# Performance work log

Hardware: AMD Instinct MI355X
Metric: run time of the kernel (lower is better)

## Reference

```python
import jax, jax.numpy as jnp
import numpy as np

# ---- module constants (from init_kwargs) ----
NOF_LINKS = 64
NOISE = 1e-3          # gen_para.input_noise_power
DT = 0.01             # gen_para.dt
T_END = 5.12          # t
TXP = 1.0             # gen_para.tx_power
LAM = 1.0
RHO = 1.0

T_ARR = jnp.arange(0.0, T_END, DT, dtype=jnp.float32)   # [T] time grid
POW2T = jnp.power(jnp.float32(2.0), T_ARR)               # 2^t
POW2T_1 = POW2T - 1.0                                    # 2^t - 1
LN2 = jnp.log(jnp.float32(2.0))


def setup_inputs() -> dict:
    key = jax.random.key(0)
    k1, k2 = jax.random.split(key)
    pathloss = jax.random.uniform(k1, (NOF_LINKS, NOF_LINKS), dtype=jnp.float32)
    powers = jax.random.uniform(k2, (16, 20, NOF_LINKS), dtype=jnp.float32)
    return {"pathloss": pathloss, "powers": powers}


def _outage(pathloss, power):
    # power: [B, N, L]; pathloss: [L, L]
    B, N, L = power.shape
    T = T_ARR.shape[0]
    # signal[b,n,i,j] = pathloss[i,j] * power[b,n,i]  (per original expand/permute)
    y_ii = jnp.diagonal(pathloss)[None, None, :] * power              # [B,N,L]
    y_tot = power * jnp.sum(pathloss, axis=1)[None, None, :]          # sum_j signal
    y_ij = y_tot - y_ii
    sinr = y_ii / (y_ij + NOISE)                                      # [B,N,L]

    # block-0 outage CDF over time grid: Q1[b,i,t] = 1 - exp(-(2^t-1) * sinr[b,0,i])
    Q1 = 1.0 - jnp.exp(-POW2T_1[None, None, :] * sinr[:, 0, :, None])  # [B,L,T]

    # per-block pdf kernels for n >= 1 (vectorized over all blocks up front)
    s = sinr[:, 1:, :, None]                                          # [B,N-1,L,1]
    q = jnp.exp(-POW2T_1 * s) * POW2T * s * LN2                       # [B,N-1,L,T]

    def step(Q, qn):
        # Q, qn: [B,L,T]; per-channel grouped cross-correlation (torch conv1d semantics)
        x = Q.reshape(1, B * L, T)
        w = qn.reshape(B * L, 1, T)
        out = jax.lax.conv_general_dilated(
            x, w, window_strides=(1,), padding=[(T - 1, T - 1)],
            feature_group_count=B * L)                                 # [1,B*L,2T-1]
        Qn = out[0, :, :T].reshape(B, L, T) * DT
        return Qn, Qn[:, :, -1]

    q_scan = jnp.moveaxis(q, 1, 0)                                    # [N-1,B,L,T]
    _, outa_rest = jax.lax.scan(step, Q1, q_scan)                     # [N-1,B,L]
    outa = jnp.concatenate([Q1[None, :, :, -1], outa_rest], axis=0)   # [N,B,L]
    return jnp.moveaxis(outa, 0, 1)                                   # [B,N,L]


def reference(pathloss, powers):
    power = powers * TXP
    N = power.shape[1]
    outa = _outage(pathloss, power)                                   # [B,N,L]
    E = power[:, 0, :] + jnp.sum(power[:, 1:, :] * outa[:, :N - 1, :], axis=1)
    D = 1.0 + jnp.sum(outa[:, :N - 1, :], axis=1)
    loss = jnp.sum(E) + LAM * jnp.sum(outa[:, N - 1, :]) + RHO * jnp.sum(D)
    return loss
```

## Files before the change

### kernel.cpp

```cpp
#include <hip/hip_runtime.h>

#define LL 64
#define NN 20
#define DTC 0.01f
#define NOISEC 1e-3f
#define LN2C 0.69314718056f
#define LOG2E 1.44269504089f

typedef __attribute__((ext_vector_type(8))) short short8x;
typedef __attribute__((ext_vector_type(4))) float f32x4;

__device__ __forceinline__ unsigned cvt_pk_bf16(float x, float y) {
    unsigned r;
    asm("v_cvt_pk_bf16_f32 %0, %1, %2" : "=v"(r) : "v"(x), "v"(y));
    return r;
}

__global__ __launch_bounds__(64, 1) void outage_kernel(
    const float* __restrict__ pathloss,
    const float* __restrict__ powers,
    float* __restrict__ out)
{
    __shared__ __align__(16) unsigned short gt[2][8][544];
    __shared__ __align__(16) unsigned short Qb[2][1024];

    const int lane = threadIdx.x;
    const int c = blockIdx.x, b = c >> 6, l = c & 63;
    const int nh = lane & 15;
    const int qd = lane >> 4;

    const float pl = pathloss[l * LL + lane];
    float rs = pl;
    #pragma unroll
    for (int mk = 1; mk < 64; mk <<= 1) rs += __shfl_xor(rs, mk, 64);
    const float dg   = __shfl(pl, l, 64);
    const float dsum = rs - dg;

    float P2[8], P1L[8];
    #pragma unroll
    for (int u = 0; u < 8; ++u) {
        float e = __builtin_amdgcn_exp2f((8 * lane + u) * DTC);
        P2[u]  = e;
        P1L[u] = (1.f - e) * LOG2E;
    }

    *((uint4*)&Qb[0][0] + lane) = uint4{0u, 0u, 0u, 0u};
    *((uint4*)&Qb[1][0] + lane) = uint4{0u, 0u, 0u, 0u};
    {
        const int bb = lane >> 5, w = lane & 31;
        #pragma unroll
        for (int k = 0; k < 8; ++k) gt[bb][k][512 + w] = 0;
    }

    const float p0 = powers[(b * NN + 0) * LL + l];
    const float s0 = dg * p0 / (p0 * dsum + NOISEC);
    float q7;
    {
        float v[8];
        #pragma unroll
        for (int u = 0; u < 8; ++u) v[u] = 1.f - __builtin_amdgcn_exp2f(P1L[u] * s0);
        q7 = v[7];
        uint4 d4 = { cvt_pk_bf16(v[0], v[1]), cvt_pk_bf16(v[2], v[3]),
                     cvt_pk_bf16(v[4], v[5]), cvt_pk_bf16(v[6], v[7]) };
        *(uint4*)&Qb[0][512 + 8 * lane] = d4;
    }

    const float p1v = powers[(b * NN + 1) * LL + l];
    float lossCh = 1.f + p0 + (p1v + 1.f) * q7;

    auto fill_g = [&](int buf, float p) {
        float s  = dg * p / (p * dsum + NOISEC);
        float cm = s * LN2C * DTC;
        unsigned F[8];
        #pragma unroll
        for (int w = 0; w < 4; ++w) {
            float a  = __builtin_amdgcn_exp2f(P1L[2 * w]     * s) * (P2[2 * w]     * cm);
            float bb = __builtin_amdgcn_exp2f(P1L[2 * w + 1] * s) * (P2[2 * w + 1] * cm);
            F[w] = cvt_pk_bf16(a, bb);
        }
        #pragma unroll
        for (int w = 0; w < 4; ++w) {
            unsigned t = (unsigned)__shfl_down((int)F[w], 1, 64);
            F[4 + w] = (lane == 63) ? 0u : t;
        }
        unsigned E[7];
        #pragma unroll
        for (int j = 0; j < 7; ++j) E[j] = __builtin_amdgcn_alignbit(F[j + 1], F[j], 16);
        #pragma unroll
        for (int k = 0; k < 8; ++k) {
            uint4 d4;
            if ((k & 1) == 0) d4 = uint4{F[k / 2], F[k / 2 + 1], F[k / 2 + 2], F[k / 2 + 3]};
            else              d4 = uint4{E[k / 2], E[k / 2 + 1], E[k / 2 + 2], E[k / 2 + 3]};
            *(uint4*)&gt[buf][k][8 * lane] = d4;
        }
    };
    fill_g(1, p1v);

    const int kk    = (7 - nh) & 7;
    const int baseA = 511 - nh + 8 * qd - kk;
    const int baseB = 512 + 32 * nh + 8 * qd;
    const int dstw  = 512 + 32 * nh + 4 * qd;

    float pnext = powers[(b * NN + 2) * LL + l];

    short8x Bv[16], A0v[16], A1v[16];
    {
        const unsigned short* pg1 = &gt[1][kk][0];
        #pragma unroll
        for (int d = 0; d < 16; ++d) {
            Bv[d]  = *(const short8x*)&Qb[0][baseB - 32 * d];
            A0v[d] = *(const short8x*)&pg1[baseA - 32 * d];
            A1v[d] = *(const short8x*)&pg1[baseA - 32 * d - 16];
        }
    }

    for (int n = 1; n < NN; ++n) {
        unsigned short* pdst = &Qb[n & 1][0];

        float pfut = 0.f;
        if (n <= NN - 3) pfut = powers[(b * NN + n + 2) * LL + l];

        if (n < NN - 1) fill_g((n + 1) & 1, pnext);

        f32x4 acc0a = {0.f, 0.f, 0.f, 0.f}, acc0b = {0.f, 0.f, 0.f, 0.f};
        f32x4 acc1a = {0.f, 0.f, 0.f, 0.f}, acc1b = {0.f, 0.f, 0.f, 0.f};
        #pragma unroll
        for (int d = 0; d < 16; d += 2) {
            acc0a = __builtin_amdgcn_mfma_f32_16x16x32_bf16(A0v[d],     Bv[d],     acc0a, 0, 0, 0);
            acc1a = __builtin_amdgcn_mfma_f32_16x16x32_bf16(A1v[d],     Bv[d],     acc1a, 0, 0, 0);
            acc0b = __builtin_amdgcn_mfma_f32_16x16x32_bf16(A0v[d + 1], Bv[d + 1], acc0b, 0, 0, 0);
            acc1b = __builtin_amdgcn_mfma_f32_16x16x32_bf16(A1v[d + 1], Bv[d + 1], acc1b, 0, 0, 0);
        }
        f32x4 acc0 = acc0a + acc0b;
        f32x4 acc1 = acc1a + acc1b;

        *(uint2*)&pdst[dstw]      = uint2{cvt_pk_bf16(acc0.x, acc0.y), cvt_pk_bf16(acc0.z, acc0.w)};
        *(uint2*)&pdst[dstw + 16] = uint2{cvt_pk_bf16(acc1.x, acc1.y), cvt_pk_bf16(acc1.z, acc1.w)};

        if (n < NN - 1) {
            const unsigned short* pgn = &gt[(n + 1) & 1][kk][0];
            #pragma unroll
            for (int d = 0; d < 16; ++d) {
                Bv[d]  = *(const short8x*)&pdst[baseB - 32 * d];
                A0v[d] = *(const short8x*)&pgn[baseA - 32 * d];
                A1v[d] = *(const short8x*)&pgn[baseA - 32 * d - 16];
            }
        }

        float wgt = (n < NN - 1) ? (pnext + 1.f) : 1.f;
        lossCh += wgt * acc1.w;
        pnext = pfut;
    }

    if (lane == 63) atomicAdd(out, lossCh);
}

extern "C" void kernel_launch(void* const* d_in, const int* in_sizes, int n_in,
                              void* d_out, int out_size, void* d_ws, size_t ws_size,
                              hipStream_t stream) {
    const float* pathloss = (const float*)d_in[0];
    const float* powers   = (const float*)d_in[1];
    float* outp = (float*)d_out;

    (void)hipMemsetAsync(d_out, 0, sizeof(float) * out_size, stream);
    outage_kernel<<<16 * LL, 64, 0, stream>>>(pathloss, powers, outp);
}
```

Measured before the change: 85.93 us.

## Process two batches per wavefront and build shifted B operands via DPP

Each workgroup now handles two batch rows (b and b+8) for the same link, halving the grid and sharing the pathloss reduction and exponent tables. The two independent convolution chains are interleaved so MFMA work of one can overlap LDS loads and kernel fills of the other. Instead of loading 16 shifted B fragments from LDS, one fragment is loaded and the other 15 are produced with DPP row-shift-right operations, cutting LDS reads. It adds register pressure, and row-shift semantics must match the original 32-element-stride loads exactly or results change.

```diff
diff --git a/kernel.cpp b/kernel.cpp
--- a/kernel.cpp
+++ b/kernel.cpp
@@ -7,25 +7,57 @@
 #define LN2C 0.69314718056f
 #define LOG2E 1.44269504089f
 
+#define GROW 552
+
 typedef __attribute__((ext_vector_type(8))) short short8x;
 typedef __attribute__((ext_vector_type(4))) float f32x4;
+typedef __attribute__((ext_vector_type(4))) int v4i;
 
 __device__ __forceinline__ unsigned cvt_pk_bf16(float x, float y) {
     unsigned r;
     asm("v_cvt_pk_bf16_f32 %0, %1, %2" : "=v"(r) : "v"(x), "v"(y));
     return r;
 }
+
+template<int CTRL>
+__device__ __forceinline__ short8x dpp_shr(short8x v) {
+    v4i p = __builtin_bit_cast(v4i, v);
+    v4i q;
+    q.x = __builtin_amdgcn_update_dpp(0, p.x, CTRL, 0xf, 0xf, true);
+    q.y = __builtin_amdgcn_update_dpp(0, p.y, CTRL, 0xf, 0xf, true);
+    q.z = __builtin_amdgcn_update_dpp(0, p.z, CTRL, 0xf, 0xf, true);
+    q.w = __builtin_amdgcn_update_dpp(0, p.w, CTRL, 0xf, 0xf, true);
+    return __builtin_bit_cast(short8x, q);
+}
+
+#define DPP_EXPAND(B)                         \
+    B[1]  = dpp_shr<0x111>(B[0]);             \
+    B[2]  = dpp_shr<0x112>(B[0]);             \
+    B[3]  = dpp_shr<0x113>(B[0]);             \
+    B[4]  = dpp_shr<0x114>(B[0]);             \
+    B[5]  = dpp_shr<0x115>(B[0]);             \
+    B[6]  = dpp_shr<0x116>(B[0]);             \
+    B[7]  = dpp_shr<0x117>(B[0]);             \
+    B[8]  = dpp_shr<0x118>(B[0]);             \
+    B[9]  = dpp_shr<0x119>(B[0]);             \
+    B[10] = dpp_shr<0x11A>(B[0]);             \
+    B[11] = dpp_shr<0x11B>(B[0]);             \
+    B[12] = dpp_shr<0x11C>(B[0]);             \
+    B[13] = dpp_shr<0x11D>(B[0]);             \
+    B[14] = dpp_shr<0x11E>(B[0]);             \
+    B[15] = dpp_shr<0x11F>(B[0]);
 
 __global__ __launch_bounds__(64, 1) void outage_kernel(
     const float* __restrict__ pathloss,
     const float* __restrict__ powers,
     float* __restrict__ out)
 {
-    __shared__ __align__(16) unsigned short gt[2][8][544];
-    __shared__ __align__(16) unsigned short Qb[2][1024];
+    __shared__ __align__(16) unsigned short gt[2][2][8][GROW];
+    __shared__ __align__(16) unsigned short Qb[2][2][1024];
 
     const int lane = threadIdx.x;
-    const int c = blockIdx.x, b = c >> 6, l = c & 63;
+    const int c0 = blockIdx.x, b0 = c0 >> 6, l = c0 & 63;
+    const int b1 = b0 + 8;
     const int nh = lane & 15;
     const int qd = lane >> 4;
 
@@ -44,31 +76,43 @@
         P1L[u] = (1.f - e) * LOG2E;
     }
 
-    *((uint4*)&Qb[0][0] + lane) = uint4{0u, 0u, 0u, 0u};
-    *((uint4*)&Qb[1][0] + lane) = uint4{0u, 0u, 0u, 0u};
+    *((uint4*)&Qb[0][0][0] + lane) = uint4{0u, 0u, 0u, 0u};
+    *((uint4*)&Qb[0][1][0] + lane) = uint4{0u, 0u, 0u, 0u};
+    *((uint4*)&Qb[1][0][0] + lane) = uint4{0u, 0u, 0u, 0u};
+    *((uint4*)&Qb[1][1][0] + lane) = uint4{0u, 0u, 0u, 0u};
     {
         const int bb = lane >> 5, w = lane & 31;
         #pragma unroll
-        for (int k = 0; k < 8; ++k) gt[bb][k][512 + w] = 0;
-    }
-
-    const float p0 = powers[(b * NN + 0) * LL + l];
-    const float s0 = dg * p0 / (p0 * dsum + NOISEC);
-    float q7;
+        for (int k = 0; k < 8; ++k) { gt[0][bb][k][512 + w] = 0; gt[1][bb][k][512 + w] = 0; }
+    }
+
+    const float p00 = powers[(b0 * NN + 0) * LL + l];
+    const float p01 = powers[(b1 * NN + 0) * LL + l];
+    const float s00 = dg * p00 / (p00 * dsum + NOISEC);
+    const float s01 = dg * p01 / (p01 * dsum + NOISEC);
+    float q70, q71;
     {
-        float v[8];
-        #pragma unroll
-        for (int u = 0; u < 8; ++u) v[u] = 1.f - __builtin_amdgcn_exp2f(P1L[u] * s0);
-        q7 = v[7];
-        uint4 d4 = { cvt_pk_bf16(v[0], v[1]), cvt_pk_bf16(v[2], v[3]),
+        float v[8], w[8];
+        #pragma unroll
+        for (int u = 0; u < 8; ++u) {
+            v[u] = 1.f - __builtin_amdgcn_exp2f(P1L[u] * s00);
+            w[u] = 1.f - __builtin_amdgcn_exp2f(P1L[u] * s01);
+        }
+        q70 = v[7]; q71 = w[7];
+        uint4 d0 = { cvt_pk_bf16(v[0], v[1]), cvt_pk_bf16(v[2], v[3]),
                      cvt_pk_bf16(v[4], v[5]), cvt_pk_bf16(v[6], v[7]) };
-        *(uint4*)&Qb[0][512 + 8 * lane] = d4;
-    }
-
-    const float p1v = powers[(b * NN + 1) * LL + l];
-    float lossCh = 1.f + p0 + (p1v + 1.f) * q7;
-
-    auto fill_g = [&](int buf, float p) {
+        uint4 d1 = { cvt_pk_bf16(w[0], w[1]), cvt_pk_bf16(w[2], w[3]),
+                     cvt_pk_bf16(w[4], w[5]), cvt_pk_bf16(w[6], w[7]) };
+        *(uint4*)&Qb[0][0][512 + 8 * lane] = d0;
+        *(uint4*)&Qb[1][0][512 + 8 * lane] = d1;
+    }
+
+    const float p1v0 = powers[(b0 * NN + 1) * LL + l];
+    const float p1v1 = powers[(b1 * NN + 1) * LL + l];
+    float loss0 = 1.f + p00 + (p1v0 + 1.f) * q70;
+    float loss1 = 1.f + p01 + (p1v1 + 1.f) * q71;
+
+    auto fill_g = [&](unsigned short* gtb, float p) {
         float s  = dg * p / (p * dsum + NOISEC);
         float cm = s * LN2C * DTC;
         unsigned F[8];
@@ -91,68 +135,96 @@
             uint4 d4;
             if ((k & 1) == 0) d4 = uint4{F[k / 2], F[k / 2 + 1], F[k / 2 + 2], F[k / 2 + 3]};
             else              d4 = uint4{E[k / 2], E[k / 2 + 1], E[k / 2 + 2], E[k / 2 + 3]};
-            *(uint4*)&gt[buf][k][8 * lane] = d4;
+            *(uint4*)&gtb[k * GROW + 8 * lane] = d4;
         }
     };
-    fill_g(1, p1v);
+    fill_g(&gt[0][1][0][0], p1v0);
+    fill_g(&gt[1][1][0][0], p1v1);
 
     const int kk    = (7 - nh) & 7;
     const int baseA = 511 - nh + 8 * qd - kk;
     const int baseB = 512 + 32 * nh + 8 * qd;
     const int dstw  = 512 + 32 * nh + 4 * qd;
 
-    float pnext = powers[(b * NN + 2) * LL + l];
-
-    short8x Bv[16], A0v[16], A1v[16];
-    {
-        const unsigned short* pg1 = &gt[1][kk][0];
+    float pn0 = powers[(b0 * NN + 2) * LL + l];
+    float pn1 = powers[(b1 * NN + 2) * LL + l];
+
+    for (int n = 1; n < NN; ++n) {
+        const int bufO = (n + 1) & 1, bufN = n & 1;
+        const unsigned short* psrc0 = &Qb[0][bufO][0];
+        const unsigned short* psrc1 = &Qb[1][bufO][0];
+        const unsigned short* pg0   = &gt[0][bufN][kk][0];
+        const unsigned short* pg1   = &gt[1][bufN][kk][0];
+        unsigned short* pdst0       = &Qb[0][bufN][0];
+        unsigned short* pdst1       = &Qb[1][bufN][0];
+
+        float pf0 = 0.f, pf1 = 0.f;
+        if (n <= NN - 3) {
+            pf0 = powers[(b0 * NN + n + 2) * LL + l];
+            pf1 = powers[(b1 * NN + n + 2) * LL + l];
+        }
+
+        short8x B0[16], B1[16];
+        B0[0] = *(const short8x*)&psrc0[baseB];
+        B1[0] = *(const short8x*)&psrc1[baseB];
+        DPP_EXPAND(B0)
+
+        short8x A00[16], A01[16];
         #pragma unroll
         for (int d = 0; d < 16; ++d) {
-            Bv[d]  = *(const short8x*)&Qb[0][baseB - 32 * d];
-            A0v[d] = *(const short8x*)&pg1[baseA - 32 * d];
-            A1v[d] = *(const short8x*)&pg1[baseA - 32 * d - 16];
-        }
-    }
-
-    for (int n = 1; n < NN; ++n) {
-        unsigned short* pdst = &Qb[n & 1][0];
-
-        float pfut = 0.f;
-        if (n <= NN - 3) pfut = powers[(b * NN + n + 2) * LL + l];
-
-        if (n < NN - 1) fill_g((n + 1) & 1, pnext);
-
-        f32x4 acc0a = {0.f, 0.f, 0.f, 0.f}, acc0b = {0.f, 0.f, 0.f, 0.f};
-        f32x4 acc1a = {0.f, 0.f, 0.f, 0.f}, acc1b = {0.f, 0.f, 0.f, 0.f};
+            A00[d] = *(const short8x*)&pg0[baseA - 32 * d];
+            A01[d] = *(const short8x*)&pg0[baseA - 32 * d - 16];
+        }
+
+        if (n < NN - 1) {
+            fill_g(&gt[0][bufO][0][0], pn0);
+            fill_g(&gt[1][bufO][0][0], pn1);
+        }
+
+        short8x A10[16], A11[16];
+        #pragma unroll
+        for (int d = 0; d < 16; ++d) {
+            A10[d] = *(const short8x*)&pg1[baseA - 32 * d];
+            A11[d] = *(const short8x*)&pg1[baseA - 32 * d - 16];
+        }
+
+        f32x4 c0a = {0.f,0.f,0.f,0.f}, c0b = {0.f,0.f,0.f,0.f};
+        f32x4 c1a = {0.f,0.f,0.f,0.f}, c1b = {0.f,0.f,0.f,0.f};
         #pragma unroll
         for (int d = 0; d < 16; d += 2) {
-            acc0a = __builtin_amdgcn_mfma_f32_16x16x32_bf16(A0v[d],     Bv[d],     acc0a, 0, 0, 0);
-            acc1a = __builtin_amdgcn_mfma_f32_16x16x32_bf16(A1v[d],     Bv[d],     acc1a, 0, 0, 0);
-            acc0b = __builtin_amdgcn_mfma_f32_16x16x32_bf16(A0v[d + 1], Bv[d + 1], acc0b, 0, 0, 0);
-            acc1b = __builtin_amdgcn_mfma_f32_16x16x32_bf16(A1v[d + 1], Bv[d + 1], acc1b, 0, 0, 0);
-        }
-        f32x4 acc0 = acc0a + acc0b;
-        f32x4 acc1 = acc1a + acc1b;
-
-        *(uint2*)&pdst[dstw]      = uint2{cvt_pk_bf16(acc0.x, acc0.y), cvt_pk_bf16(acc0.z, acc0.w)};
-        *(uint2*)&pdst[dstw + 16] = uint2{cvt_pk_bf16(acc1.x, acc1.y), cvt_pk_bf16(acc1.z, acc1.w)};
-
-        if (n < NN - 1) {
-            const unsigned short* pgn = &gt[(n + 1) & 1][kk][0];
-            #pragma unroll
-            for (int d = 0; d < 16; ++d) {
-                Bv[d]  = *(const short8x*)&pdst[baseB - 32 * d];
-                A0v[d] = *(const short8x*)&pgn[baseA - 32 * d];
-                A1v[d] = *(const short8x*)&pgn[baseA - 32 * d - 16];
-            }
-        }
-
-        float wgt = (n < NN - 1) ? (pnext + 1.f) : 1.f;
-        lossCh += wgt * acc1.w;
-        pnext = pfut;
-    }
-
-    if (lane == 63) atomicAdd(out, lossCh);
+            c0a = __builtin_amdgcn_mfma_f32_16x16x32_bf16(A00[d],     B0[d],     c0a, 0, 0, 0);
+            c1a = __builtin_amdgcn_mfma_f32_16x16x32_bf16(A01[d],     B0[d],     c1a, 0, 0, 0);
+            c0b = __builtin_amdgcn_mfma_f32_16x16x32_bf16(A00[d + 1], B0[d + 1], c0b, 0, 0, 0);
+            c1b = __builtin_amdgcn_mfma_f32_16x16x32_bf16(A01[d + 1], B0[d + 1], c1b, 0, 0, 0);
+        }
+        f32x4 acc00 = c0a + c0b;
+        f32x4 acc01 = c1a + c1b;
+        *(uint2*)&pdst0[dstw]      = uint2{cvt_pk_bf16(acc00.x, acc00.y), cvt_pk_bf16(acc00.z, acc00.w)};
+        *(uint2*)&pdst0[dstw + 16] = uint2{cvt_pk_bf16(acc01.x, acc01.y), cvt_pk_bf16(acc01.z, acc01.w)};
+
+        DPP_EXPAND(B1)
+        f32x4 d0a = {0.f,0.f,0.f,0.f}, d0b = {0.f,0.f,0.f,0.f};
+        f32x4 d1a = {0.f,0.f,0.f,0.f}, d1b = {0.f,0.f,0.f,0.f};
+        #pragma unroll
+        for (int d = 0; d < 16; d += 2) {
+            d0a = __builtin_amdgcn_mfma_f32_16x16x32_bf16(A10[d],     B1[d],     d0a, 0, 0, 0);
+            d1a = __builtin_amdgcn_mfma_f32_16x16x32_bf16(A11[d],     B1[d],     d1a, 0, 0, 0);
+            d0b = __builtin_amdgcn_mfma_f32_16x16x32_bf16(A10[d + 1], B1[d + 1], d0b, 0, 0, 0);
+            d1b = __builtin_amdgcn_mfma_f32_16x16x32_bf16(A11[d + 1], B1[d + 1], d1b, 0, 0, 0);
+        }
+        f32x4 acc10 = d0a + d0b;
+        f32x4 acc11 = d1a + d1b;
+        *(uint2*)&pdst1[dstw]      = uint2{cvt_pk_bf16(acc10.x, acc10.y), cvt_pk_bf16(acc10.z, acc10.w)};
+        *(uint2*)&pdst1[dstw + 16] = uint2{cvt_pk_bf16(acc11.x, acc11.y), cvt_pk_bf16(acc11.z, acc11.w)};
+
+        float w0 = (n < NN - 1) ? (pn0 + 1.f) : 1.f;
+        float w1 = (n < NN - 1) ? (pn1 + 1.f) : 1.f;
+        loss0 += w0 * acc01.w;
+        loss1 += w1 * acc11.w;
+        pn0 = pf0; pn1 = pf1;
+    }
+
+    if (lane == 63) atomicAdd(out, loss0 + loss1);
 }
 
 extern "C" void kernel_launch(void* const* d_in, const int* in_sizes, int n_in,
@@ -163,5 +235,5 @@
     float* outp = (float*)d_out;
 
     (void)hipMemsetAsync(d_out, 0, sizeof(float) * out_size, stream);
-    outage_kernel<<<16 * LL, 64, 0, stream>>>(pathloss, powers, outp);
-}
+    outage_kernel<<<8 * LL, 64, 0, stream>>>(pathloss, powers, outp);
+}
```

After: 90.97 us. 1.06x slower.
